# Kernel tuning notes

Measured on AMD Instinct MI355X. Metric: run time of the kernel, lower is better.

## Reference

```python
import jax, jax.numpy as jnp
import numpy as np

B, N, DIM = 4, 2048, 1024
HEADS, DIM_HEAD = 16, 64
INNER = HEADS * DIM_HEAD  # 1024
SCALE = DIM_HEAD ** -0.5


def setup_inputs() -> dict:
    key = jax.random.key(0)
    k_x, k_qkv, k_out, k_b = jax.random.split(key, 4)
    x = jax.random.normal(k_x, (B, N, DIM), dtype=jnp.float32)
    # nn.Linear weights, stored transposed for x @ W convenience
    w_qkv = jax.random.normal(k_qkv, (DIM, 3 * INNER), dtype=jnp.float32) * (DIM ** -0.5)
    w_out = jax.random.normal(k_out, (INNER, DIM), dtype=jnp.float32) * (INNER ** -0.5)
    b_out = jax.random.normal(k_b, (DIM,), dtype=jnp.float32) * 0.01
    return {"x": x, "w_qkv": w_qkv, "w_out": w_out, "b_out": b_out}


def _split_heads(t):
    # 'b n (h d) -> (b h) n d'
    b, n, _ = t.shape
    return t.reshape(b, n, HEADS, DIM_HEAD).transpose(0, 2, 1, 3).reshape(b * HEADS, n, DIM_HEAD)


def reference(x, w_qkv, w_out, b_out):
    b, n, _ = x.shape
    qkv = x @ w_qkv  # [b, n, 3*inner]
    q, k, v = jnp.split(qkv, 3, axis=-1)
    q = q * SCALE
    q, k, v = map(_split_heads, (q, k, v))  # [(b h), n, d]
    sim = jnp.einsum('bid,bjd->bij', q, k)  # [(b h), n, n]
    a = jax.nn.softmax(sim, axis=-1)
    out = jnp.einsum('bij,bjd->bid', a, v)  # [(b h), n, d]
    # '(b h) n d -> b n (h d)'
    out = out.reshape(b, HEADS, n, DIM_HEAD).transpose(0, 2, 1, 3).reshape(b, n, INNER)
    return out @ w_out + b_out  # dropout p=0.0 is identity
```

## Files before the change

### kernel.cpp

```cpp
#include <hip/hip_runtime.h>
#include <stdint.h>


typedef uint16_t u16;
typedef __bf16 bf16x8 __attribute__((ext_vector_type(8)));
typedef float f32x4 __attribute__((ext_vector_type(4)));
typedef unsigned u32x2 __attribute__((ext_vector_type(2)));
typedef unsigned u32x4 __attribute__((ext_vector_type(4)));

#define AS3(p) ((__attribute__((address_space(3))) uint32_t*)(p))
#define AS1(p) ((const __attribute__((address_space(1))) uint32_t*)(p))

__device__ __forceinline__ void gl_lds16(const void* g, void* lds) {
  __builtin_amdgcn_global_load_lds(AS1(g), AS3(lds), 16, 0, 0);
}

__device__ __forceinline__ u16 f2bf(float f) {
  union { __bf16 b; u16 u; } x; x.b = (__bf16)f;
  return x.u;
}

__global__ void cvt_f32_bf16(const float* __restrict__ in, u16* __restrict__ out, long n) {
  long i = ((long)blockIdx.x * 256 + threadIdx.x) * 8;
  if (i >= n) return;
  u16 r[8];
  #pragma unroll
  for (int j = 0; j < 8; ++j) r[j] = f2bf(in[i + j]);
  *(uint4*)(out + i) = *(const uint4*)r;
}

__global__ void transpose_f2b(const float* __restrict__ in, u16* __restrict__ out, int R, int C) {
  __shared__ u16 tile[32][33];
  int tx = threadIdx.x, ty = threadIdx.y;
  int c0 = blockIdx.x * 32, r0 = blockIdx.y * 32;
  #pragma unroll
  for (int i = 0; i < 4; ++i)
    tile[ty + 8 * i][tx] = f2bf(in[(long)(r0 + ty + 8 * i) * C + c0 + tx]);
  __syncthreads();
  #pragma unroll
  for (int i = 0; i < 4; ++i)
    out[(long)(c0 + ty + 8 * i) * R + r0 + tx] = tile[tx][ty + 8 * i];
}

template <bool BIAS, bool OUTF32>
__global__ __launch_bounds__(256) void gemm_bt(const u16* __restrict__ A, const u16* __restrict__ Bt,
                                               const float* __restrict__ bias, void* __restrict__ Cv,
                                               int M, int N, int K, int qcols, float qscale) {
  __shared__ u16 sA[128 * 32];
  __shared__ u16 sB[128 * 32];
  const int tid = threadIdx.x;
  const int w = tid >> 6, l = tid & 63;
  const int l15 = l & 15, lh = l >> 4;
  const int wr = w >> 1, wc = w & 1;
  const long row0 = (long)blockIdx.y * 128, col0 = (long)blockIdx.x * 128;

  const f32x4 fzero = {0.f, 0.f, 0.f, 0.f};
  f32x4 acc[4][4];
  #pragma unroll
  for (int m = 0; m < 4; ++m)
    #pragma unroll
    for (int n = 0; n < 4; ++n) acc[m][n] = fzero;

  for (int kt = 0; kt < K; kt += 32) {
    __syncthreads();
    #pragma unroll
    for (int i = 0; i < 2; ++i) {
      int c = w * 128 + i * 64 + l;
      gl_lds16(A + (row0 + (c >> 2)) * K + kt + (c & 3) * 8,
               (void*)(sA + (w * 128 + i * 64) * 8));
      gl_lds16(Bt + (col0 + (c >> 2)) * K + kt + (c & 3) * 8,
               (void*)(sB + (w * 128 + i * 64) * 8));
    }
    __syncthreads();
    bf16x8 a[4], b[4];
    #pragma unroll
    for (int m = 0; m < 4; ++m)
      a[m] = *(const bf16x8*)&sA[(wr * 64 + m * 16 + l15) * 32 + lh * 8];
    #pragma unroll
    for (int n = 0; n < 4; ++n)
      b[n] = *(const bf16x8*)&sB[(wc * 64 + n * 16 + l15) * 32 + lh * 8];
    #pragma unroll
    for (int m = 0; m < 4; ++m)
      #pragma unroll
      for (int n = 0; n < 4; ++n)
        acc[m][n] = __builtin_amdgcn_mfma_f32_16x16x32_bf16(a[m], b[n], acc[m][n], 0, 0, 0);
  }

  #pragma unroll
  for (int n = 0; n < 4; ++n) {
    long col = col0 + wc * 64 + n * 16 + l15;
    float bv = 0.f;
    if (BIAS) bv = bias[col];
    float scl = (col < qcols) ? qscale : 1.0f;
    #pragma unroll
    for (int m = 0; m < 4; ++m) {
      #pragma unroll
      for (int r = 0; r < 4; ++r) {
        long row = row0 + wr * 64 + m * 16 + lh * 4 + r;
        if (OUTF32) ((float*)Cv)[row * N + col] = acc[m][n][r] + bv;
        else        ((u16*)Cv)[row * N + col] = f2bf(acc[m][n][r] * scl + bv);
      }
    }
  }
}

__global__ __launch_bounds__(512, 4) void attn_k(const u16* __restrict__ qkv, u16* __restrict__ attn) {
  __shared__ u16 smem[24576];
  const int tid = threadIdx.x;
  const int w = tid >> 6, l = tid & 63;
  const int l15 = l & 15, lh = l >> 4;
  const int b = blockIdx.x >> 4, h = blockIdx.x & 15;
  const int qt = blockIdx.y;
  const long rs = 3072;
  const long qrow0 = (long)b * 2048 + qt * 256;
  const u16* Qg    = qkv + qrow0 * rs + h * 64;
  const u16* Kbase = qkv + (long)b * 2048 * rs + 1024 + h * 64;
  const u16* Vbase = qkv + (long)b * 2048 * rs + 2048 + h * 64;

  #pragma unroll
  for (int i = 0; i < 4; ++i) {
    int c = (w * 4 + i) * 64 + l;
    int row = c >> 3;
    int col8 = ((c & 7) ^ (row & 7)) * 8;
    gl_lds16(Qg + (long)row * rs + col8, (void*)(smem + (w * 4 + i) * 512));
  }
  {
    int c = tid;
    int row = c >> 3;
    int col8 = ((c & 7) ^ (row & 7)) * 8;
    gl_lds16(Kbase + (long)row * rs + col8, (void*)(smem + 16384 + w * 512));

    int kv0 = (tid & 31) * 2, d0 = (tid >> 5) * 4;
    const u16* Vg = Vbase + (long)kv0 * rs + d0;
    u32x2 va = *(const u32x2*)Vg;
    u32x2 vb = *(const u32x2*)(Vg + rs);
    const u16* pa = (const u16*)&va;
    const u16* pb = (const u16*)&vb;
    #pragma unroll
    for (int jj = 0; jj < 4; ++jj) {
      int d = d0 + jj;
      *(uint32_t*)&smem[20480 + d * 64 + (kv0 ^ ((d & 7) << 3))] =
          (uint32_t)pa[jj] | ((uint32_t)pb[jj] << 16);
    }
  }
  __syncthreads();

  bf16x8 aq[2][2];
  #pragma unroll
  for (int m = 0; m < 2; ++m)
    #pragma unroll
    for (int ks = 0; ks < 2; ++ks) {
      int row = w * 32 + m * 16 + l15;
      aq[m][ks] = *(const bf16x8*)&smem[row * 64 + ((ks * 32 + lh * 8) ^ ((row & 7) << 3))];
    }
  __syncthreads();

  bf16x8 ones;
  { union { u32x4 u; bf16x8 f; } cv; cv.u = (u32x4){0x3F803F80u, 0x3F803F80u, 0x3F803F80u, 0x3F803F80u}; ones = cv.f; }

  const f32x4 fzero = {0.f, 0.f, 0.f, 0.f};
  f32x4 acc[2][4];
  f32x4 acc_l[2];
  #pragma unroll
  for (int m = 0; m < 2; ++m) {
    acc_l[m] = fzero;
    #pragma unroll
    for (int n = 0; n < 4; ++n) acc[m][n] = fzero;
  }

  for (int t = 0; t < 32; ++t) {
    const int kOff  = (t & 1) ? 0     : 16384;
    const int vOff  = (t & 1) ? 4096  : 20480;
    const int kOffN = (t & 1) ? 16384 : 0;
    const int vOffN = (t & 1) ? 20480 : 4096;

    f32x4 s[2][4];
    #pragma unroll
    for (int m = 0; m < 2; ++m)
      #pragma unroll
      for (int n = 0; n < 4; ++n) s[m][n] = fzero;
    #pragma unroll
    for (int ks = 0; ks < 2; ++ks) {
      bf16x8 bk[4];
      #pragma unroll
      for (int n = 0; n < 4; ++n) {
        int row = n * 16 + l15;
        bk[n] = *(const bf16x8*)&smem[kOff + row * 64 + ((ks * 32 + lh * 8) ^ ((row & 7) << 3))];
      }
      __builtin_amdgcn_s_setprio(1);
      #pragma unroll
      for (int m = 0; m < 2; ++m)
        #pragma unroll
        for (int n = 0; n < 4; ++n)
          s[m][n] = __builtin_amdgcn_mfma_f32_16x16x32_bf16(bk[n], aq[m][ks], s[m][n], 0, 0, 0);
      __builtin_amdgcn_s_setprio(0);
    }

    uint4 kreg;
    u32x2 va, vb;
    int kv0 = (tid & 31) * 2, d0v = (tid >> 5) * 4;
    if (t < 31) {
      int row = tid >> 3, sub = tid & 7;
      kreg = *(const uint4*)(Kbase + ((long)(t + 1) * 64 + row) * rs + sub * 8);
      const u16* Vg = Vbase + ((long)(t + 1) * 64 + kv0) * rs + d0v;
      va = *(const u32x2*)Vg;
      vb = *(const u32x2*)(Vg + rs);
    }

    unsigned Wm[2][4][2];
    #pragma unroll
    for (int m = 0; m < 2; ++m) {
      #pragma unroll
      for (int n = 0; n < 4; ++n) {
        float p0 = __builtin_amdgcn_exp2f(s[m][n][0]);
        float p1 = __builtin_amdgcn_exp2f(s[m][n][1]);
        float p2 = __builtin_amdgcn_exp2f(s[m][n][2]);
        float p3 = __builtin_amdgcn_exp2f(s[m][n][3]);
        Wm[m][n][0] = (unsigned)f2bf(p0) | ((unsigned)f2bf(p1) << 16);
        Wm[m][n][1] = (unsigned)f2bf(p2) | ((unsigned)f2bf(p3) << 16);
      }
    }

    #pragma unroll
    for (int ks = 0; ks < 2; ++ks) {
      bf16x8 pf[2];
      #pragma unroll
      for (int m = 0; m < 2; ++m) {
        unsigned a0 = Wm[m][2 * ks][0], b0 = Wm[m][2 * ks + 1][0];
        unsigned a1 = Wm[m][2 * ks][1], b1 = Wm[m][2 * ks + 1][1];
        asm("v_permlane32_swap_b32 %0, %1" : "+v"(a0), "+v"(b0));
        asm("v_permlane16_swap_b32 %0, %1" : "+v"(a0), "+v"(b0));
        asm("v_permlane32_swap_b32 %0, %1" : "+v"(a1), "+v"(b1));
        asm("v_permlane16_swap_b32 %0, %1" : "+v"(a1), "+v"(b1));
        union { u32x4 u; bf16x8 f; } cv;
        cv.u = (u32x4){a0, a1, b0, b1};
        pf[m] = cv.f;
      }
      bf16x8 bv4[4];
      #pragma unroll
      for (int n = 0; n < 4; ++n) {
        int vr = n * 16 + l15;
        bv4[n] = *(const bf16x8*)&smem[vOff + vr * 64 + ((ks * 32 + lh * 8) ^ ((vr & 7) << 3))];
      }
      __builtin_amdgcn_s_setprio(1);
      #pragma unroll
      for (int n = 0; n < 4; ++n)
        #pragma unroll
        for (int m = 0; m < 2; ++m)
          acc[m][n] = __builtin_amdgcn_mfma_f32_16x16x32_bf16(bv4[n], pf[m], acc[m][n], 0, 0, 0);
      #pragma unroll
      for (int m = 0; m < 2; ++m)
        acc_l[m] = __builtin_amdgcn_mfma_f32_16x16x32_bf16(ones, pf[m], acc_l[m], 0, 0, 0);
      __builtin_amdgcn_s_setprio(0);
    }

    if (t < 31) {
      int row = tid >> 3, sub = tid & 7;
      *(uint4*)&smem[kOffN + row * 64 + (sub ^ (row & 7)) * 8] = kreg;
      const u16* pa = (const u16*)&va;
      const u16* pb = (const u16*)&vb;
      #pragma unroll
      for (int jj = 0; jj < 4; ++jj) {
        int d = d0v + jj;
        *(uint32_t*)&smem[vOffN + d * 64 + (kv0 ^ ((d & 7) << 3))] =
            (uint32_t)pa[jj] | ((uint32_t)pb[jj] << 16);
      }
      __syncthreads();
    }
  }

  #pragma unroll
  for (int m = 0; m < 2; ++m) {
    float inv = 1.0f / acc_l[m][0];
    long q = qrow0 + w * 32 + m * 16 + l15;
    #pragma unroll
    for (int n = 0; n < 4; ++n) {
      unsigned lo = (unsigned)f2bf(acc[m][n][0] * inv) | ((unsigned)f2bf(acc[m][n][1] * inv) << 16);
      unsigned hi = (unsigned)f2bf(acc[m][n][2] * inv) | ((unsigned)f2bf(acc[m][n][3] * inv) << 16);
      *(u32x2*)&attn[q * 1024 + h * 64 + n * 16 + lh * 4] = (u32x2){lo, hi};
    }
  }
}

extern "C" void kernel_launch(void* const* d_in, const int* in_sizes, int n_in,
                              void* d_out, int out_size, void* d_ws, size_t ws_size,
                              hipStream_t stream) {
  (void)in_sizes; (void)n_in; (void)out_size; (void)ws_size;
  const float* x     = (const float*)d_in[0];
  const float* w_qkv = (const float*)d_in[1];
  const float* w_out = (const float*)d_in[2];
  const float* b_out = (const float*)d_in[3];
  float* out = (float*)d_out;

  u16* ws    = (u16*)d_ws;
  u16* wqkvT = ws;
  u16* woutT = wqkvT + (size_t)3072 * 1024;
  u16* xbf   = woutT + (size_t)1024 * 1024;
  u16* qkv   = xbf   + (size_t)8192 * 1024;
  u16* attnb = qkv   + (size_t)8192 * 3072;

  const float QSCALE = 0.125f * 1.44269504088896f;

  cvt_f32_bf16<<<4096, 256, 0, stream>>>(x, xbf, (long)8192 * 1024);
  transpose_f2b<<<dim3(96, 32), dim3(32, 8), 0, stream>>>(w_qkv, wqkvT, 1024, 3072);
  transpose_f2b<<<dim3(32, 32), dim3(32, 8), 0, stream>>>(w_out, woutT, 1024, 1024);
  gemm_bt<false, false><<<dim3(24, 64), 256, 0, stream>>>(xbf, wqkvT, nullptr, qkv,
                                                          8192, 3072, 1024, 1024, QSCALE);
  attn_k<<<dim3(64, 8), 512, 0, stream>>>(qkv, attnb);
  gemm_bt<true, true><<<dim3(8, 64), 256, 0, stream>>>(attnb, woutT, b_out, out,
                                                       8192, 1024, 1024, 0, 1.0f);
}
```

Measured before the change: 197.1 us.

## Widen GEMM K-tile with swizzled LDS, remap blocks per XCD, async K prefetch

The GEMM now loads 64-wide K tiles into XOR-swizzled LDS and issues two MFMA sub-steps per barrier, halving the number of syncs. Block indices are remapped so that consecutive row tiles land on the same XCD, which should improve L2 reuse. The attention kernel now prefetches the next K tile directly into LDS with global_load_lds instead of staging it through registers. The two weight transposes are merged into one launch. LDS usage doubles in the GEMM, and the earlier async K write must not race with readers of the other buffer.

Result: faster. 190.4 us (-3.4%).

```diff
diff --git a/kernel.cpp b/kernel.cpp
--- a/kernel.cpp
+++ b/kernel.cpp
@@ -29,10 +29,18 @@
   *(uint4*)(out + i) = *(const uint4*)r;
 }
 
-__global__ void transpose_f2b(const float* __restrict__ in, u16* __restrict__ out, int R, int C) {
+__global__ void transpose2_f2b(const float* __restrict__ in0, u16* __restrict__ out0,
+                               const float* __restrict__ in1, u16* __restrict__ out1,
+                               int C0, int C1) {
+  const int R = 1024;
+  const float* in = blockIdx.z ? in1 : in0;
+  u16* out = blockIdx.z ? out1 : out0;
+  int C = blockIdx.z ? C1 : C0;
+  int c0 = blockIdx.x * 32;
+  if (c0 >= C) return;
   __shared__ u16 tile[32][33];
   int tx = threadIdx.x, ty = threadIdx.y;
-  int c0 = blockIdx.x * 32, r0 = blockIdx.y * 32;
+  int r0 = blockIdx.y * 32;
   #pragma unroll
   for (int i = 0; i < 4; ++i)
     tile[ty + 8 * i][tx] = f2bf(in[(long)(r0 + ty + 8 * i) * C + c0 + tx]);
@@ -46,13 +54,17 @@
 __global__ __launch_bounds__(256) void gemm_bt(const u16* __restrict__ A, const u16* __restrict__ Bt,
                                                const float* __restrict__ bias, void* __restrict__ Cv,
                                                int M, int N, int K, int qcols, float qscale) {
-  __shared__ u16 sA[128 * 32];
-  __shared__ u16 sB[128 * 32];
+  __shared__ u16 sA[128 * 64];
+  __shared__ u16 sB[128 * 64];
   const int tid = threadIdx.x;
   const int w = tid >> 6, l = tid & 63;
   const int l15 = l & 15, lh = l >> 4;
   const int wr = w >> 1, wc = w & 1;
-  const long row0 = (long)blockIdx.y * 128, col0 = (long)blockIdx.x * 128;
+  int bid = blockIdx.x + blockIdx.y * gridDim.x;
+  int xcd = bid & 7, idx = bid >> 3;
+  int by = xcd * (gridDim.y >> 3) + idx / gridDim.x;
+  int bx = idx % gridDim.x;
+  const long row0 = (long)by * 128, col0 = (long)bx * 128;
 
   const f32x4 fzero = {0.f, 0.f, 0.f, 0.f};
   f32x4 acc[4][4];
@@ -61,29 +73,38 @@
     #pragma unroll
     for (int n = 0; n < 4; ++n) acc[m][n] = fzero;
 
-  for (int kt = 0; kt < K; kt += 32) {
+  for (int kt = 0; kt < K; kt += 64) {
     __syncthreads();
     #pragma unroll
-    for (int i = 0; i < 2; ++i) {
-      int c = w * 128 + i * 64 + l;
-      gl_lds16(A + (row0 + (c >> 2)) * K + kt + (c & 3) * 8,
-               (void*)(sA + (w * 128 + i * 64) * 8));
-      gl_lds16(Bt + (col0 + (c >> 2)) * K + kt + (c & 3) * 8,
-               (void*)(sB + (w * 128 + i * 64) * 8));
+    for (int i = 0; i < 4; ++i) {
+      int c = w * 256 + i * 64 + l;
+      int row = c >> 3, sub = c & 7;
+      int col8 = (sub ^ (row & 7)) * 8;
+      gl_lds16(A + (row0 + row) * K + kt + col8, (void*)(sA + w * 2048 + i * 512));
+      gl_lds16(Bt + (col0 + row) * K + kt + col8, (void*)(sB + w * 2048 + i * 512));
     }
     __syncthreads();
-    bf16x8 a[4], b[4];
-    #pragma unroll
-    for (int m = 0; m < 4; ++m)
-      a[m] = *(const bf16x8*)&sA[(wr * 64 + m * 16 + l15) * 32 + lh * 8];
-    #pragma unroll
-    for (int n = 0; n < 4; ++n)
-      b[n] = *(const bf16x8*)&sB[(wc * 64 + n * 16 + l15) * 32 + lh * 8];
-    #pragma unroll
-    for (int m = 0; m < 4; ++m)
-      #pragma unroll
-      for (int n = 0; n < 4; ++n)
-        acc[m][n] = __builtin_amdgcn_mfma_f32_16x16x32_bf16(a[m], b[n], acc[m][n], 0, 0, 0);
+    #pragma unroll
+    for (int ks = 0; ks < 2; ++ks) {
+      bf16x8 a[4], b[4];
+      #pragma unroll
+      for (int m = 0; m < 4; ++m) {
+        int row = wr * 64 + m * 16 + l15;
+        a[m] = *(const bf16x8*)&sA[row * 64 + ((ks * 32 + lh * 8) ^ ((row & 7) << 3))];
+      }
+      #pragma unroll
+      for (int n = 0; n < 4; ++n) {
+        int row = wc * 64 + n * 16 + l15;
+        b[n] = *(const bf16x8*)&sB[row * 64 + ((ks * 32 + lh * 8) ^ ((row & 7) << 3))];
+      }
+      __builtin_amdgcn_s_setprio(1);
+      #pragma unroll
+      for (int m = 0; m < 4; ++m)
+        #pragma unroll
+        for (int n = 0; n < 4; ++n)
+          acc[m][n] = __builtin_amdgcn_mfma_f32_16x16x32_bf16(a[m], b[n], acc[m][n], 0, 0, 0);
+      __builtin_amdgcn_s_setprio(0);
+    }
   }
 
   #pragma unroll
@@ -125,9 +146,8 @@
     gl_lds16(Qg + (long)row * rs + col8, (void*)(smem + (w * 4 + i) * 512));
   }
   {
-    int c = tid;
-    int row = c >> 3;
-    int col8 = ((c & 7) ^ (row & 7)) * 8;
+    int row = tid >> 3, sub = tid & 7;
+    int col8 = (sub ^ (row & 7)) * 8;
     gl_lds16(Kbase + (long)row * rs + col8, (void*)(smem + 16384 + w * 512));
 
     int kv0 = (tid & 31) * 2, d0 = (tid >> 5) * 4;
@@ -174,6 +194,17 @@
     const int kOffN = (t & 1) ? 16384 : 0;
     const int vOffN = (t & 1) ? 20480 : 4096;
 
+    u32x2 va, vb;
+    int kv0 = (tid & 31) * 2, d0v = (tid >> 5) * 4;
+    if (t < 31) {
+      int row = tid >> 3, sub = tid & 7;
+      int col8 = (sub ^ (row & 7)) * 8;
+      gl_lds16(Kbase + ((long)(t + 1) * 64 + row) * rs + col8, (void*)(smem + kOffN + w * 512));
+      const u16* Vg = Vbase + ((long)(t + 1) * 64 + kv0) * rs + d0v;
+      va = *(const u32x2*)Vg;
+      vb = *(const u32x2*)(Vg + rs);
+    }
+
     f32x4 s[2][4];
     #pragma unroll
     for (int m = 0; m < 2; ++m)
@@ -194,17 +225,6 @@
         for (int n = 0; n < 4; ++n)
           s[m][n] = __builtin_amdgcn_mfma_f32_16x16x32_bf16(bk[n], aq[m][ks], s[m][n], 0, 0, 0);
       __builtin_amdgcn_s_setprio(0);
-    }
-
-    uint4 kreg;
-    u32x2 va, vb;
-    int kv0 = (tid & 31) * 2, d0v = (tid >> 5) * 4;
-    if (t < 31) {
-      int row = tid >> 3, sub = tid & 7;
-      kreg = *(const uint4*)(Kbase + ((long)(t + 1) * 64 + row) * rs + sub * 8);
-      const u16* Vg = Vbase + ((long)(t + 1) * 64 + kv0) * rs + d0v;
-      va = *(const u32x2*)Vg;
-      vb = *(const u32x2*)(Vg + rs);
     }
 
     unsigned Wm[2][4][2];
@@ -255,8 +275,6 @@
     }
 
     if (t < 31) {
-      int row = tid >> 3, sub = tid & 7;
-      *(uint4*)&smem[kOffN + row * 64 + (sub ^ (row & 7)) * 8] = kreg;
       const u16* pa = (const u16*)&va;
       const u16* pb = (const u16*)&vb;
       #pragma unroll
@@ -302,8 +320,7 @@
   const float QSCALE = 0.125f * 1.44269504088896f;
 
   cvt_f32_bf16<<<4096, 256, 0, stream>>>(x, xbf, (long)8192 * 1024);
-  transpose_f2b<<<dim3(96, 32), dim3(32, 8), 0, stream>>>(w_qkv, wqkvT, 1024, 3072);
-  transpose_f2b<<<dim3(32, 32), dim3(32, 8), 0, stream>>>(w_out, woutT, 1024, 1024);
+  transpose2_f2b<<<dim3(96, 32, 2), dim3(32, 8), 0, stream>>>(w_qkv, wqkvT, w_out, woutT, 3072, 1024);
   gemm_bt<false, false><<<dim3(24, 64), 256, 0, stream>>>(xbf, wqkvT, nullptr, qkv,
                                                           8192, 3072, 1024, 1024, QSCALE);
   attn_k<<<dim3(64, 8), 512, 0, stream>>>(qkv, attnb);
```
